# Kernel tuning notes

Measured on AMD Instinct MI355X. Metric: run time of the kernel, lower is better.

The kernel has to match this reference:

```python
import jax, jax.numpy as jnp
import numpy as np

B, T, C = 4, 2048, 1024
H, D = 16, 64
SCALE = D ** -0.5


def setup_inputs() -> dict:
    key = jax.random.key(0)
    ks = jax.random.split(key, 5)
    s = 0.02
    return {
        "hidden_states": jax.random.normal(ks[0], (B, T, C), dtype=jnp.float32),
        "attention_mask": jnp.ones((B, T), dtype=jnp.int32),
        "Wq": jax.random.normal(ks[1], (C, H * D), dtype=jnp.float32) * s,
        "Wk": jax.random.normal(ks[2], (C, H * D), dtype=jnp.float32) * s,
        "Wv": jax.random.normal(ks[3], (C, H * D), dtype=jnp.float32) * s,
        "Wo": jax.random.normal(ks[4], (H * D, C), dtype=jnp.float32) * s,
        "bo": jnp.zeros((C,), dtype=jnp.float32),
    }


def reference(hidden_states, attention_mask, Wq, Wk, Wv, Wo, bo):
    b, t, _ = hidden_states.shape
    # projections -> (B, H, T, D)
    q = (hidden_states @ Wq).reshape(b, t, H, D).transpose(0, 2, 1, 3)
    k = (hidden_states @ Wk).reshape(b, t, H, D).transpose(0, 2, 1, 3)
    v = (hidden_states @ Wv).reshape(b, t, H, D).transpose(0, 2, 1, 3)
    # scores (B, H, Tq, Tk)
    scores = jnp.einsum("bhqd,bhkd->bhqk", q, k) * SCALE
    mask = attention_mask[:, None, None, :]  # (B,1,1,T), dim==2 branch
    scores = jnp.where(mask == 0, -jnp.inf, scores)
    probs = jax.nn.softmax(scores, axis=-1)
    out = jnp.einsum("bhqk,bhkd->bhqd", probs, v)
    out = out.transpose(0, 2, 1, 3).reshape(b, t, H * D)
    return out @ Wo + bo
```

## Files before the change

kernel.cpp:

```cpp
#include <hip/hip_runtime.h>
#include <hip/hip_bf16.h>

#define B_ 4
#define T_ 2048
#define C_ 1024
#define H_ 16
#define D_ 64
#define SCALE_ 0.125f
#define L2E 1.4426950408889634f
#define SE (SCALE_ * L2E)

typedef __attribute__((ext_vector_type(8))) short bf16x8;
typedef __attribute__((ext_vector_type(4))) float f32x4;

__device__ __forceinline__ unsigned short f2bf(float f) {
    union { float f; unsigned u; } v; v.f = f;
    unsigned r = v.u + 0x7fff + ((v.u >> 16) & 1);
    return (unsigned short)(r >> 16);
}

__device__ __forceinline__ unsigned pk2bf(float a, float b) {
    __hip_bfloat162 t = __float22bfloat162_rn(make_float2(a, b));
    union { __hip_bfloat162 h; unsigned u; } c; c.h = t;
    return c.u;
}

__device__ __forceinline__ void gl_lds16(const unsigned short* g, unsigned short* l) {
    __builtin_amdgcn_global_load_lds(
        (const __attribute__((address_space(1))) void*)g,
        (__attribute__((address_space(3))) void*)l,
        16, 0, 0);
}

__global__ void cvt_hs_kernel(const float4* __restrict__ in, ushort4* __restrict__ out) {
    int i = blockIdx.x * 256 + threadIdx.x;
    float4 v = in[i];
    ushort4 o;
    o.x = f2bf(v.x); o.y = f2bf(v.y); o.z = f2bf(v.z); o.w = f2bf(v.w);
    out[i] = o;
}

__global__ void wtrans_kernel(const float* __restrict__ Wq, const float* __restrict__ Wk,
                              const float* __restrict__ Wv, const float* __restrict__ Wo,
                              unsigned short* __restrict__ Wqkv_t, unsigned short* __restrict__ Wo_t) {
    __shared__ float tile[64][65];
    int mtx = blockIdx.y;
    const float* W = (mtx == 0) ? Wq : (mtx == 1) ? Wk : (mtx == 2) ? Wv : Wo;
    unsigned short* Out = (mtx < 3) ? (Wqkv_t + (size_t)mtx * 1024 * 1024) : Wo_t;
    int tl = blockIdx.x;
    int tx = tl & 15, ty = tl >> 4;
    int t = threadIdx.x;
    int col = t & 63, rb = t >> 6;
#pragma unroll
    for (int rr = 0; rr < 16; ++rr) {
        int r = rb * 16 + rr;
        tile[r][col] = W[(size_t)(ty * 64 + r) * 1024 + tx * 64 + col];
    }
    __syncthreads();
#pragma unroll
    for (int rr = 0; rr < 16; ++rr) {
        int r = rb * 16 + rr;
        Out[(size_t)(tx * 64 + r) * 1024 + ty * 64 + col] = f2bf(tile[col][r]);
    }
}

__global__ __launch_bounds__(256) void gemm_qkv_kernel(
    const unsigned short* __restrict__ A, const unsigned short* __restrict__ Bt,
    unsigned short* __restrict__ Qg, unsigned short* __restrict__ Kf, unsigned short* __restrict__ Vf) {
    __shared__ __align__(16) unsigned short As[128 * 32];
    __shared__ __align__(16) unsigned short Bs[128 * 32];
    const int tid = threadIdx.x;
    const int w = tid >> 6, lane = tid & 63;
    const int quad = lane >> 4, l16 = lane & 15;
    const int m0 = blockIdx.y * 128, n0 = blockIdx.x * 128;
    const int mw = (w >> 1) * 64, nw = (w & 1) * 64;
    const int K = 1024;
    const int srow = lane >> 2;
    const int scol = (lane & 3) * 8;

    const f32x4 fzero = {0.f, 0.f, 0.f, 0.f};
    f32x4 acc[4][4];
#pragma unroll
    for (int i = 0; i < 4; ++i)
#pragma unroll
        for (int j = 0; j < 4; ++j) acc[i][j] = fzero;

    for (int k0 = 0; k0 < K; k0 += 32) {
        gl_lds16(A + (size_t)(m0 + w * 32 + srow) * K + k0 + scol,       As + (w * 32) * 32);
        gl_lds16(A + (size_t)(m0 + w * 32 + 16 + srow) * K + k0 + scol,  As + (w * 32 + 16) * 32);
        gl_lds16(Bt + (size_t)(n0 + w * 32 + srow) * K + k0 + scol,      Bs + (w * 32) * 32);
        gl_lds16(Bt + (size_t)(n0 + w * 32 + 16 + srow) * K + k0 + scol, Bs + (w * 32 + 16) * 32);
        __syncthreads();
        bf16x8 a[4], b[4];
#pragma unroll
        for (int i = 0; i < 4; ++i)
            a[i] = *(const bf16x8*)(As + (mw + i * 16 + l16) * 32 + quad * 8);
#pragma unroll
        for (int j = 0; j < 4; ++j)
            b[j] = *(const bf16x8*)(Bs + (nw + j * 16 + l16) * 32 + quad * 8);
#pragma unroll
        for (int i = 0; i < 4; ++i)
#pragma unroll
            for (int j = 0; j < 4; ++j)
                acc[i][j] = __builtin_amdgcn_mfma_f32_16x16x32_bf16(a[i], b[j], acc[i][j], 0, 0, 0);
        __syncthreads();
    }

#pragma unroll
    for (int j = 0; j < 4; ++j) {
        int gn = n0 + nw + j * 16 + l16;
        int tensor = gn >> 10;
        int nl = gn & 1023;
        int hh = nl >> 6, dd = nl & 63;
#pragma unroll
        for (int i = 0; i < 4; ++i) {
            int gmb = m0 + mw + i * 16 + quad * 4;
            int bb = gmb >> 11;
            size_t bhh = (size_t)(bb * 16 + hh);
            if (tensor == 0) {
#pragma unroll
                for (int r = 0; r < 4; ++r) {
                    int tt = (gmb + r) & 2047;
                    Qg[(bhh * 2048 + tt) * 64 + dd] = f2bf(acc[i][j][r] * SE);
                }
            } else if (tensor == 1) {
#pragma unroll
                for (int r = 0; r < 4; ++r) {
                    int tt = (gmb + r) & 2047;
                    Kf[bhh * 131072 + (size_t)(tt >> 4) * 1024 + (dd >> 5) * 512 +
                       (((dd >> 3) & 3) * 16 + (tt & 15)) * 8 + (dd & 7)] = f2bf(acc[i][j][r]);
                }
            } else {
                int tt = gmb & 2047;
                ushort4 v4;
                v4.x = f2bf(acc[i][j][0]); v4.y = f2bf(acc[i][j][1]);
                v4.z = f2bf(acc[i][j][2]); v4.w = f2bf(acc[i][j][3]);
                *(ushort4*)(Vf + bhh * 131072 + (size_t)(tt >> 5) * 2048 + (dd >> 4) * 512 +
                            (((tt >> 3) & 3) * 16 + (dd & 15)) * 8 + (tt & 7)) = v4;
            }
        }
    }
}

__global__ __launch_bounds__(256) void attn_kernel(
    const unsigned short* __restrict__ Qg, const unsigned short* __restrict__ Kf,
    const unsigned short* __restrict__ Vf, const int* __restrict__ mask,
    unsigned short* __restrict__ AO) {
    __shared__ __align__(16) unsigned short Pbuf[4][2048];

    const int tid = threadIdx.x;
    const int w = tid >> 6, lane = tid & 63;
    const int quad = lane >> 4, l16 = lane & 15;
    const int bid = blockIdx.x;
    const int bh = (bid & 7) * 8 + ((bid >> 7) & 7);
    const int qt = (bid >> 3) & 15;
    const int b = bh >> 4, h = bh & 15;
    const size_t bh_td = (size_t)bh * (2048 * 64);
    const int q0w = qt * 128 + w * 32;

    bf16x8 aq[2][2];
#pragma unroll
    for (int qi = 0; qi < 2; ++qi)
#pragma unroll
        for (int hh = 0; hh < 2; ++hh)
            aq[qi][hh] = *(const bf16x8*)(Qg + bh_td + (size_t)(q0w + qi * 16 + l16) * 64 + hh * 32 + quad * 8);

    const unsigned short* Kp = Kf + bh_td + lane * 8;
    const unsigned short* Vp = Vf + bh_td + lane * 8;
    const int* mrow = mask + b * 2048;

    bf16x8 vones;
#pragma unroll
    for (int i = 0; i < 8; ++i) vones[i] = (short)0x3F80;

    const f32x4 fzero = {0.f, 0.f, 0.f, 0.f};
    f32x4 po[2][4];
    f32x4 pl[2];
#pragma unroll
    for (int qi = 0; qi < 2; ++qi) {
        pl[qi] = fzero;
#pragma unroll
        for (int nd = 0; nd < 4; ++nd) po[qi][nd] = fzero;
    }

    for (int k0 = 0; k0 < 2048; k0 += 64) {
        const int tb = (k0 >> 4) * 1024;
        bf16x8 ka0[4], ka1[4];
#pragma unroll
        for (int kt = 0; kt < 4; ++kt) {
            ka0[kt] = *(const bf16x8*)(Kp + tb + kt * 1024);
            ka1[kt] = *(const bf16x8*)(Kp + tb + kt * 1024 + 512);
        }

        int mk = mrow[k0 + lane];
        bool allok = (__ballot(mk != 0) == 0xFFFFFFFFFFFFFFFFull);

        if (allok) {
#pragma unroll
            for (int kt = 0; kt < 4; ++kt) {
                int pidx = ((((kt & 1) << 1) | (quad >> 1)) * 16 + l16) * 8 + (quad & 1) * 4;
#pragma unroll
                for (int qi = 0; qi < 2; ++qi) {
                    f32x4 st = __builtin_amdgcn_mfma_f32_16x16x32_bf16(ka0[kt], aq[qi][0], fzero, 0, 0, 0);
                    st = __builtin_amdgcn_mfma_f32_16x16x32_bf16(ka1[kt], aq[qi][1], st, 0, 0, 0);
                    float p0 = __builtin_amdgcn_exp2f(st[0]);
                    float p1 = __builtin_amdgcn_exp2f(st[1]);
                    float p2 = __builtin_amdgcn_exp2f(st[2]);
                    float p3 = __builtin_amdgcn_exp2f(st[3]);
                    uint2 pk; pk.x = pk2bf(p0, p1); pk.y = pk2bf(p2, p3);
                    *(uint2*)(Pbuf[w] + (qi * 2 + (kt >> 1)) * 512 + pidx) = pk;
                }
            }
        } else {
#pragma unroll
            for (int kt = 0; kt < 4; ++kt) {
                int4 mv = *(const int4*)(mrow + k0 + kt * 16 + quad * 4);
                float mb0 = mv.x ? 0.f : -1e30f;
                float mb1 = mv.y ? 0.f : -1e30f;
                float mb2 = mv.z ? 0.f : -1e30f;
                float mb3 = mv.w ? 0.f : -1e30f;
                int pidx = ((((kt & 1) << 1) | (quad >> 1)) * 16 + l16) * 8 + (quad & 1) * 4;
#pragma unroll
                for (int qi = 0; qi < 2; ++qi) {
                    f32x4 st = __builtin_amdgcn_mfma_f32_16x16x32_bf16(ka0[kt], aq[qi][0], fzero, 0, 0, 0);
                    st = __builtin_amdgcn_mfma_f32_16x16x32_bf16(ka1[kt], aq[qi][1], st, 0, 0, 0);
                    float p0 = __builtin_amdgcn_exp2f(st[0] + mb0);
                    float p1 = __builtin_amdgcn_exp2f(st[1] + mb1);
                    float p2 = __builtin_amdgcn_exp2f(st[2] + mb2);
                    float p3 = __builtin_amdgcn_exp2f(st[3] + mb3);
                    uint2 pk; pk.x = pk2bf(p0, p1); pk.y = pk2bf(p2, p3);
                    *(uint2*)(Pbuf[w] + (qi * 2 + (kt >> 1)) * 512 + pidx) = pk;
                }
            }
        }

        bf16x8 bv[2][4];
#pragma unroll
        for (int c = 0; c < 2; ++c)
#pragma unroll
            for (int nd = 0; nd < 4; ++nd)
                bv[c][nd] = *(const bf16x8*)(Vp + ((k0 >> 5) + c) * 2048 + nd * 512);

        asm volatile("s_waitcnt lgkmcnt(0)" ::: "memory");

#pragma unroll
        for (int c = 0; c < 2; ++c)
#pragma unroll
            for (int qi = 0; qi < 2; ++qi) {
                bf16x8 ap = *(const bf16x8*)(Pbuf[w] + (qi * 2 + c) * 512 + lane * 8);
#pragma unroll
                for (int nd = 0; nd < 4; ++nd)
                    po[qi][nd] = __builtin_amdgcn_mfma_f32_16x16x32_bf16(ap, bv[c][nd], po[qi][nd], 0, 0, 0);
                pl[qi] = __builtin_amdgcn_mfma_f32_16x16x32_bf16(ap, vones, pl[qi], 0, 0, 0);
            }
    }

#pragma unroll
    for (int qi = 0; qi < 2; ++qi)
#pragma unroll
        for (int r = 0; r < 4; ++r) {
            float linv = __builtin_amdgcn_rcpf(pl[qi][r]);
            int q = q0w + qi * 16 + quad * 4 + r;
            size_t ob = (size_t)(b * 2048 + q) * 1024 + h * 64;
#pragma unroll
            for (int nd = 0; nd < 4; ++nd)
                AO[ob + nd * 16 + l16] = f2bf(po[qi][nd][r] * linv);
        }
}

__global__ __launch_bounds__(256) void gemm_out_kernel(
    const unsigned short* __restrict__ A, const unsigned short* __restrict__ Bt,
    const float* __restrict__ bo, float* __restrict__ out) {
    __shared__ __align__(16) unsigned short As[128 * 32];
    __shared__ __align__(16) unsigned short Bs[128 * 32];
    const int tid = threadIdx.x;
    const int w = tid >> 6, lane = tid & 63;
    const int quad = lane >> 4, l16 = lane & 15;
    const int m0 = blockIdx.y * 128, n0 = blockIdx.x * 128;
    const int mw = (w >> 1) * 64, nw = (w & 1) * 64;
    const int K = 1024;
    const int srow = lane >> 2;
    const int scol = (lane & 3) * 8;

    const f32x4 fzero = {0.f, 0.f, 0.f, 0.f};
    f32x4 acc[4][4];
#pragma unroll
    for (int i = 0; i < 4; ++i)
#pragma unroll
        for (int j = 0; j < 4; ++j) acc[i][j] = fzero;

    for (int k0 = 0; k0 < K; k0 += 32) {
        gl_lds16(A + (size_t)(m0 + w * 32 + srow) * K + k0 + scol,       As + (w * 32) * 32);
        gl_lds16(A + (size_t)(m0 + w * 32 + 16 + srow) * K + k0 + scol,  As + (w * 32 + 16) * 32);
        gl_lds16(Bt + (size_t)(n0 + w * 32 + srow) * K + k0 + scol,      Bs + (w * 32) * 32);
        gl_lds16(Bt + (size_t)(n0 + w * 32 + 16 + srow) * K + k0 + scol, Bs + (w * 32 + 16) * 32);
        __syncthreads();
        bf16x8 a[4], b[4];
#pragma unroll
        for (int i = 0; i < 4; ++i)
            a[i] = *(const bf16x8*)(As + (mw + i * 16 + l16) * 32 + quad * 8);
#pragma unroll
        for (int j = 0; j < 4; ++j)
            b[j] = *(const bf16x8*)(Bs + (nw + j * 16 + l16) * 32 + quad * 8);
#pragma unroll
        for (int i = 0; i < 4; ++i)
#pragma unroll
            for (int j = 0; j < 4; ++j)
                acc[i][j] = __builtin_amdgcn_mfma_f32_16x16x32_bf16(a[i], b[j], acc[i][j], 0, 0, 0);
        __syncthreads();
    }

#pragma unroll
    for (int j = 0; j < 4; ++j) {
        int gn = n0 + nw + j * 16 + l16;
        float bias = bo[gn];
#pragma unroll
        for (int i = 0; i < 4; ++i) {
            int gmb = m0 + mw + i * 16 + quad * 4;
#pragma unroll
            for (int r = 0; r < 4; ++r)
                out[(size_t)(gmb + r) * 1024 + gn] = acc[i][j][r] + bias;
        }
    }
}

extern "C" void kernel_launch(void* const* d_in, const int* in_sizes, int n_in,
                              void* d_out, int out_size, void* d_ws, size_t ws_size,
                              hipStream_t stream) {
    const float* hs  = (const float*)d_in[0];
    const int* mask  = (const int*)d_in[1];
    const float* Wq  = (const float*)d_in[2];
    const float* Wk  = (const float*)d_in[3];
    const float* Wv  = (const float*)d_in[4];
    const float* Wo  = (const float*)d_in[5];
    const float* bo  = (const float*)d_in[6];
    float* out = (float*)d_out;

    char* ws = (char*)d_ws;
    unsigned short* hs_bf = (unsigned short*)(ws);
    unsigned short* wqkv  = (unsigned short*)(ws + 16777216);
    unsigned short* wo_t  = (unsigned short*)(ws + 23068672);
    unsigned short* Qg    = (unsigned short*)(ws + 25165824);
    unsigned short* Kf    = (unsigned short*)(ws + 41943040);
    unsigned short* Vf    = (unsigned short*)(ws + 58720256);
    unsigned short* AO    = (unsigned short*)(ws + 75497472);

    cvt_hs_kernel<<<8192, 256, 0, stream>>>((const float4*)hs, (ushort4*)hs_bf);
    wtrans_kernel<<<dim3(256, 4), 256, 0, stream>>>(Wq, Wk, Wv, Wo, wqkv, wo_t);
    gemm_qkv_kernel<<<dim3(24, 64), 256, 0, stream>>>(hs_bf, wqkv, Qg, Kf, Vf);
    attn_kernel<<<1024, 256, 0, stream>>>(Qg, Kf, Vf, mask, AO);
    gemm_out_kernel<<<dim3(8, 64), 256, 0, stream>>>(AO, wo_t, bo, out);
}
```

Before: 294.5 us.

## Software-pipeline K loads with register double buffering and hoist mask check

Checks the whole attention mask row once up front. When no key is masked, the kernel runs a fast loop that prefetches the next K tile into a second register set while the current tile is computed, and issues the V loads before the QK MFMAs. It also raises wave priority around MFMA groups with s_setprio. This is meant to hide global load latency and drop the per-iteration ballot, at the cost of more registers and a duplicated code path. The final prefetch reads one tile past the end of K (k0+128 = 2048), which goes out of bounds for the last head.

```diff
diff --git a/kernel.cpp b/kernel.cpp
--- a/kernel.cpp
+++ b/kernel.cpp
@@ -142,6 +142,62 @@
     }
 }
 
+
+__device__ __forceinline__ void attn_step(
+    int k0, const unsigned short* __restrict__ Kp, const unsigned short* __restrict__ Vp,
+    unsigned short* Pw, const bf16x8 (&aq)[2][2],
+    const bf16x8 (&ka0)[4], const bf16x8 (&ka1)[4],
+    bf16x8 (&kn0)[4], bf16x8 (&kn1)[4], int next_tb,
+    const bf16x8& vones, f32x4 (&po)[2][4], f32x4 (&pl)[2],
+    int quad, int l16, int lane) {
+    bf16x8 bv[2][4];
+#pragma unroll
+    for (int c = 0; c < 2; ++c)
+#pragma unroll
+        for (int nd = 0; nd < 4; ++nd)
+            bv[c][nd] = *(const bf16x8*)(Vp + ((k0 >> 5) + c) * 2048 + nd * 512);
+#pragma unroll
+    for (int kt = 0; kt < 4; ++kt) {
+        kn0[kt] = *(const bf16x8*)(Kp + next_tb + kt * 1024);
+        kn1[kt] = *(const bf16x8*)(Kp + next_tb + kt * 1024 + 512);
+    }
+
+    const f32x4 fzero = {0.f, 0.f, 0.f, 0.f};
+    const int pbase = (quad >> 1) * 128 + l16 * 8 + (quad & 1) * 4;
+#pragma unroll
+    for (int kt = 0; kt < 4; ++kt) {
+        int pidx = pbase + (kt & 1) * 256;
+#pragma unroll
+        for (int qi = 0; qi < 2; ++qi) {
+            __builtin_amdgcn_s_setprio(1);
+            f32x4 st = __builtin_amdgcn_mfma_f32_16x16x32_bf16(ka0[kt], aq[qi][0], fzero, 0, 0, 0);
+            st = __builtin_amdgcn_mfma_f32_16x16x32_bf16(ka1[kt], aq[qi][1], st, 0, 0, 0);
+            __builtin_amdgcn_s_setprio(0);
+            float p0 = __builtin_amdgcn_exp2f(st[0]);
+            float p1 = __builtin_amdgcn_exp2f(st[1]);
+            float p2 = __builtin_amdgcn_exp2f(st[2]);
+            float p3 = __builtin_amdgcn_exp2f(st[3]);
+            uint2 pk; pk.x = pk2bf(p0, p1); pk.y = pk2bf(p2, p3);
+            *(uint2*)(Pw + (qi * 2 + (kt >> 1)) * 512 + pidx) = pk;
+        }
+    }
+
+    asm volatile("s_waitcnt lgkmcnt(0)" ::: "memory");
+
+#pragma unroll
+    for (int c = 0; c < 2; ++c)
+#pragma unroll
+        for (int qi = 0; qi < 2; ++qi) {
+            bf16x8 ap = *(const bf16x8*)(Pw + (qi * 2 + c) * 512 + lane * 8);
+            __builtin_amdgcn_s_setprio(1);
+#pragma unroll
+            for (int nd = 0; nd < 4; ++nd)
+                po[qi][nd] = __builtin_amdgcn_mfma_f32_16x16x32_bf16(ap, bv[c][nd], po[qi][nd], 0, 0, 0);
+            pl[qi] = __builtin_amdgcn_mfma_f32_16x16x32_bf16(ap, vones, pl[qi], 0, 0, 0);
+            __builtin_amdgcn_s_setprio(0);
+        }
+}
+
 __global__ __launch_bounds__(256) void attn_kernel(
     const unsigned short* __restrict__ Qg, const unsigned short* __restrict__ Kf,
     const unsigned short* __restrict__ Vf, const int* __restrict__ mask,
@@ -183,76 +239,100 @@
         for (int nd = 0; nd < 4; ++nd) po[qi][nd] = fzero;
     }
 
-    for (int k0 = 0; k0 < 2048; k0 += 64) {
-        const int tb = (k0 >> 4) * 1024;
-        bf16x8 ka0[4], ka1[4];
+    bool okl = true;
+#pragma unroll
+    for (int r = 0; r < 8; ++r) {
+        int4 m4 = *(const int4*)(mrow + r * 256 + lane * 4);
+        okl = okl && (m4.x != 0) && (m4.y != 0) && (m4.z != 0) && (m4.w != 0);
+    }
+    const bool all_ok = (__ballot(okl) == 0xFFFFFFFFFFFFFFFFull);
+
+    if (all_ok) {
+        bf16x8 kaA0[4], kaA1[4], kaB0[4], kaB1[4];
 #pragma unroll
         for (int kt = 0; kt < 4; ++kt) {
-            ka0[kt] = *(const bf16x8*)(Kp + tb + kt * 1024);
-            ka1[kt] = *(const bf16x8*)(Kp + tb + kt * 1024 + 512);
-        }
-
-        int mk = mrow[k0 + lane];
-        bool allok = (__ballot(mk != 0) == 0xFFFFFFFFFFFFFFFFull);
-
-        if (allok) {
+            kaA0[kt] = *(const bf16x8*)(Kp + kt * 1024);
+            kaA1[kt] = *(const bf16x8*)(Kp + kt * 1024 + 512);
+        }
+#pragma unroll 1
+        for (int k0 = 0; k0 < 2048; k0 += 128) {
+            attn_step(k0, Kp, Vp, Pbuf[w], aq, kaA0, kaA1, kaB0, kaB1,
+                      ((k0 + 64) >> 4) * 1024, vones, po, pl, quad, l16, lane);
+            attn_step(k0 + 64, Kp, Vp, Pbuf[w], aq, kaB0, kaB1, kaA0, kaA1,
+                      ((k0 + 128) >> 4) * 1024, vones, po, pl, quad, l16, lane);
+        }
+    } else {
+        for (int k0 = 0; k0 < 2048; k0 += 64) {
+            const int tb = (k0 >> 4) * 1024;
+            bf16x8 ka0[4], ka1[4];
 #pragma unroll
             for (int kt = 0; kt < 4; ++kt) {
-                int pidx = ((((kt & 1) << 1) | (quad >> 1)) * 16 + l16) * 8 + (quad & 1) * 4;
-#pragma unroll
-                for (int qi = 0; qi < 2; ++qi) {
-                    f32x4 st = __builtin_amdgcn_mfma_f32_16x16x32_bf16(ka0[kt], aq[qi][0], fzero, 0, 0, 0);
-                    st = __builtin_amdgcn_mfma_f32_16x16x32_bf16(ka1[kt], aq[qi][1], st, 0, 0, 0);
-                    float p0 = __builtin_amdgcn_exp2f(st[0]);
-                    float p1 = __builtin_amdgcn_exp2f(st[1]);
-                    float p2 = __builtin_amdgcn_exp2f(st[2]);
-                    float p3 = __builtin_amdgcn_exp2f(st[3]);
-                    uint2 pk; pk.x = pk2bf(p0, p1); pk.y = pk2bf(p2, p3);
-                    *(uint2*)(Pbuf[w] + (qi * 2 + (kt >> 1)) * 512 + pidx) = pk;
+                ka0[kt] = *(const bf16x8*)(Kp + tb + kt * 1024);
+                ka1[kt] = *(const bf16x8*)(Kp + tb + kt * 1024 + 512);
+            }
+
+            int mk = mrow[k0 + lane];
+            bool allok = (__ballot(mk != 0) == 0xFFFFFFFFFFFFFFFFull);
+
+            if (allok) {
+#pragma unroll
+                for (int kt = 0; kt < 4; ++kt) {
+                    int pidx = ((((kt & 1) << 1) | (quad >> 1)) * 16 + l16) * 8 + (quad & 1) * 4;
+#pragma unroll
+                    for (int qi = 0; qi < 2; ++qi) {
+                        f32x4 st = __builtin_amdgcn_mfma_f32_16x16x32_bf16(ka0[kt], aq[qi][0], fzero, 0, 0, 0);
+                        st = __builtin_amdgcn_mfma_f32_16x16x32_bf16(ka1[kt], aq[qi][1], st, 0, 0, 0);
+                        float p0 = __builtin_amdgcn_exp2f(st[0]);
+                        float p1 = __builtin_amdgcn_exp2f(st[1]);
+                        float p2 = __builtin_amdgcn_exp2f(st[2]);
+                        float p3 = __builtin_amdgcn_exp2f(st[3]);
+                        uint2 pk; pk.x = pk2bf(p0, p1); pk.y = pk2bf(p2, p3);
+                        *(uint2*)(Pbuf[w] + (qi * 2 + (kt >> 1)) * 512 + pidx) = pk;
+                    }
+                }
+            } else {
+#pragma unroll
+                for (int kt = 0; kt < 4; ++kt) {
+                    int4 mv = *(const int4*)(mrow + k0 + kt * 16 + quad * 4);
+                    float mb0 = mv.x ? 0.f : -1e30f;
+                    float mb1 = mv.y ? 0.f : -1e30f;
+                    float mb2 = mv.z ? 0.f : -1e30f;
+                    float mb3 = mv.w ? 0.f : -1e30f;
+                    int pidx = ((((kt & 1) << 1) | (quad >> 1)) * 16 + l16) * 8 + (quad & 1) * 4;
+#pragma unroll
+                    for (int qi = 0; qi < 2; ++qi) {
+                        f32x4 st = __builtin_amdgcn_mfma_f32_16x16x32_bf16(ka0[kt], aq[qi][0], fzero, 0, 0, 0);
+                        st = __builtin_amdgcn_mfma_f32_16x16x32_bf16(ka1[kt], aq[qi][1], st, 0, 0, 0);
+                        float p0 = __builtin_amdgcn_exp2f(st[0] + mb0);
+                        float p1 = __builtin_amdgcn_exp2f(st[1] + mb1);
+                        float p2 = __builtin_amdgcn_exp2f(st[2] + mb2);
+                        float p3 = __builtin_amdgcn_exp2f(st[3] + mb3);
+                        uint2 pk; pk.x = pk2bf(p0, p1); pk.y = pk2bf(p2, p3);
+                        *(uint2*)(Pbuf[w] + (qi * 2 + (kt >> 1)) * 512 + pidx) = pk;
+                    }
                 }
             }
-        } else {
-#pragma unroll
-            for (int kt = 0; kt < 4; ++kt) {
-                int4 mv = *(const int4*)(mrow + k0 + kt * 16 + quad * 4);
-                float mb0 = mv.x ? 0.f : -1e30f;
-                float mb1 = mv.y ? 0.f : -1e30f;
-                float mb2 = mv.z ? 0.f : -1e30f;
-                float mb3 = mv.w ? 0.f : -1e30f;
-                int pidx = ((((kt & 1) << 1) | (quad >> 1)) * 16 + l16) * 8 + (quad & 1) * 4;
+
+            bf16x8 bv[2][4];
+#pragma unroll
+            for (int c = 0; c < 2; ++c)
+#pragma unroll
+                for (int nd = 0; nd < 4; ++nd)
+                    bv[c][nd] = *(const bf16x8*)(Vp + ((k0 >> 5) + c) * 2048 + nd * 512);
+
+            asm volatile("s_waitcnt lgkmcnt(0)" ::: "memory");
+
+#pragma unroll
+            for (int c = 0; c < 2; ++c)
 #pragma unroll
                 for (int qi = 0; qi < 2; ++qi) {
-                    f32x4 st = __builtin_amdgcn_mfma_f32_16x16x32_bf16(ka0[kt], aq[qi][0], fzero, 0, 0, 0);
-                    st = __builtin_amdgcn_mfma_f32_16x16x32_bf16(ka1[kt], aq[qi][1], st, 0, 0, 0);
-                    float p0 = __builtin_amdgcn_exp2f(st[0] + mb0);
-                    float p1 = __builtin_amdgcn_exp2f(st[1] + mb1);
-                    float p2 = __builtin_amdgcn_exp2f(st[2] + mb2);
-                    float p3 = __builtin_amdgcn_exp2f(st[3] + mb3);
-                    uint2 pk; pk.x = pk2bf(p0, p1); pk.y = pk2bf(p2, p3);
-                    *(uint2*)(Pbuf[w] + (qi * 2 + (kt >> 1)) * 512 + pidx) = pk;
+                    bf16x8 ap = *(const bf16x8*)(Pbuf[w] + (qi * 2 + c) * 512 + lane * 8);
+#pragma unroll
+                    for (int nd = 0; nd < 4; ++nd)
+                        po[qi][nd] = __builtin_amdgcn_mfma_f32_16x16x32_bf16(ap, bv[c][nd], po[qi][nd], 0, 0, 0);
+                    pl[qi] = __builtin_amdgcn_mfma_f32_16x16x32_bf16(ap, vones, pl[qi], 0, 0, 0);
                 }
-            }
-        }
-
-        bf16x8 bv[2][4];
-#pragma unroll
-        for (int c = 0; c < 2; ++c)
-#pragma unroll
-            for (int nd = 0; nd < 4; ++nd)
-                bv[c][nd] = *(const bf16x8*)(Vp + ((k0 >> 5) + c) * 2048 + nd * 512);
-
-        asm volatile("s_waitcnt lgkmcnt(0)" ::: "memory");
-
-#pragma unroll
-        for (int c = 0; c < 2; ++c)
-#pragma unroll
-            for (int qi = 0; qi < 2; ++qi) {
-                bf16x8 ap = *(const bf16x8*)(Pbuf[w] + (qi * 2 + c) * 512 + lane * 8);
-#pragma unroll
-                for (int nd = 0; nd < 4; ++nd)
-                    po[qi][nd] = __builtin_amdgcn_mfma_f32_16x16x32_bf16(ap, bv[c][nd], po[qi][nd], 0, 0, 0);
-                pl[qi] = __builtin_amdgcn_mfma_f32_16x16x32_bf16(ap, vones, pl[qi], 0, 0, 0);
-            }
+        }
     }
 
 #pragma unroll
```

Result: slower. 304.5 us (+3.4%).

## Double-buffer K/V tiles in LDS and share them across 8 waves per block

Applied to the files above, without the earlier changes.

The attention kernel now uses 512-thread blocks covering 256 query rows, so eight waves share each K/V tile. Tiles are loaded into shared memory with direct global-to-LDS copies, and the next tile is prefetched into a second buffer while the current one is computed. Before, every wave read K and V straight from global memory. The aim is to cut redundant global/L2 traffic and hide load latency. In exchange it adds a block-wide barrier every 64 keys and more LDS per block, which may limit occupancy, and it halves the grid to 512 blocks.

```diff
diff --git a/kernel.cpp b/kernel.cpp
--- a/kernel.cpp
+++ b/kernel.cpp
@@ -142,21 +142,105 @@
     }
 }
 
-__global__ __launch_bounds__(256) void attn_kernel(
+__device__ __forceinline__ void attn_step_staged(
+    int k0, const unsigned short* Kc, const unsigned short* Vc,
+    unsigned short* Kn, unsigned short* Vn, int kn0,
+    const unsigned short* __restrict__ Kg, const unsigned short* __restrict__ Vg,
+    unsigned short* Pw, const bf16x8 (&aq)[2][2], const bf16x8& vones,
+    f32x4 (&po)[2][4], f32x4 (&pl)[2],
+    const int* __restrict__ mrow, int w, int lane, int quad, int l16) {
+
+    gl_lds16(Kg + (size_t)(kn0 >> 4) * 1024 + w * 512 + lane * 8, Kn + w * 512);
+    gl_lds16(Vg + (size_t)(kn0 >> 5) * 2048 + w * 512 + lane * 8, Vn + w * 512);
+
+    bf16x8 ka0[4], ka1[4];
+#pragma unroll
+    for (int kt = 0; kt < 4; ++kt) {
+        ka0[kt] = *(const bf16x8*)(Kc + kt * 1024 + lane * 8);
+        ka1[kt] = *(const bf16x8*)(Kc + kt * 1024 + 512 + lane * 8);
+    }
+
+    const f32x4 fzero = {0.f, 0.f, 0.f, 0.f};
+    int mk = mrow[k0 + lane];
+    bool allok = (__ballot(mk != 0) == 0xFFFFFFFFFFFFFFFFull);
+
+    if (allok) {
+#pragma unroll
+        for (int kt = 0; kt < 4; ++kt) {
+            int pidx = ((((kt & 1) << 1) | (quad >> 1)) * 16 + l16) * 8 + (quad & 1) * 4;
+#pragma unroll
+            for (int qi = 0; qi < 2; ++qi) {
+                f32x4 st = __builtin_amdgcn_mfma_f32_16x16x32_bf16(ka0[kt], aq[qi][0], fzero, 0, 0, 0);
+                st = __builtin_amdgcn_mfma_f32_16x16x32_bf16(ka1[kt], aq[qi][1], st, 0, 0, 0);
+                float p0 = __builtin_amdgcn_exp2f(st[0]);
+                float p1 = __builtin_amdgcn_exp2f(st[1]);
+                float p2 = __builtin_amdgcn_exp2f(st[2]);
+                float p3 = __builtin_amdgcn_exp2f(st[3]);
+                uint2 pk; pk.x = pk2bf(p0, p1); pk.y = pk2bf(p2, p3);
+                *(uint2*)(Pw + (qi * 2 + (kt >> 1)) * 512 + pidx) = pk;
+            }
+        }
+    } else {
+#pragma unroll
+        for (int kt = 0; kt < 4; ++kt) {
+            int4 mv = *(const int4*)(mrow + k0 + kt * 16 + quad * 4);
+            float mb0 = mv.x ? 0.f : -1e30f;
+            float mb1 = mv.y ? 0.f : -1e30f;
+            float mb2 = mv.z ? 0.f : -1e30f;
+            float mb3 = mv.w ? 0.f : -1e30f;
+            int pidx = ((((kt & 1) << 1) | (quad >> 1)) * 16 + l16) * 8 + (quad & 1) * 4;
+#pragma unroll
+            for (int qi = 0; qi < 2; ++qi) {
+                f32x4 st = __builtin_amdgcn_mfma_f32_16x16x32_bf16(ka0[kt], aq[qi][0], fzero, 0, 0, 0);
+                st = __builtin_amdgcn_mfma_f32_16x16x32_bf16(ka1[kt], aq[qi][1], st, 0, 0, 0);
+                float p0 = __builtin_amdgcn_exp2f(st[0] + mb0);
+                float p1 = __builtin_amdgcn_exp2f(st[1] + mb1);
+                float p2 = __builtin_amdgcn_exp2f(st[2] + mb2);
+                float p3 = __builtin_amdgcn_exp2f(st[3] + mb3);
+                uint2 pk; pk.x = pk2bf(p0, p1); pk.y = pk2bf(p2, p3);
+                *(uint2*)(Pw + (qi * 2 + (kt >> 1)) * 512 + pidx) = pk;
+            }
+        }
+    }
+
+    bf16x8 bv[2][4];
+#pragma unroll
+    for (int c = 0; c < 2; ++c)
+#pragma unroll
+        for (int nd = 0; nd < 4; ++nd)
+            bv[c][nd] = *(const bf16x8*)(Vc + c * 2048 + nd * 512 + lane * 8);
+
+    asm volatile("s_waitcnt lgkmcnt(0)" ::: "memory");
+
+#pragma unroll
+    for (int c = 0; c < 2; ++c)
+#pragma unroll
+        for (int qi = 0; qi < 2; ++qi) {
+            bf16x8 ap = *(const bf16x8*)(Pw + (qi * 2 + c) * 512 + lane * 8);
+#pragma unroll
+            for (int nd = 0; nd < 4; ++nd)
+                po[qi][nd] = __builtin_amdgcn_mfma_f32_16x16x32_bf16(ap, bv[c][nd], po[qi][nd], 0, 0, 0);
+            pl[qi] = __builtin_amdgcn_mfma_f32_16x16x32_bf16(ap, vones, pl[qi], 0, 0, 0);
+        }
+}
+
+__global__ __launch_bounds__(512, 4) void attn_kernel(
     const unsigned short* __restrict__ Qg, const unsigned short* __restrict__ Kf,
     const unsigned short* __restrict__ Vf, const int* __restrict__ mask,
     unsigned short* __restrict__ AO) {
-    __shared__ __align__(16) unsigned short Pbuf[4][2048];
+    __shared__ __align__(16) unsigned short KsA[4096], KsB[4096];
+    __shared__ __align__(16) unsigned short VsA[4096], VsB[4096];
+    __shared__ __align__(16) unsigned short Pbuf[8][2048];
 
     const int tid = threadIdx.x;
     const int w = tid >> 6, lane = tid & 63;
     const int quad = lane >> 4, l16 = lane & 15;
     const int bid = blockIdx.x;
-    const int bh = (bid & 7) * 8 + ((bid >> 7) & 7);
-    const int qt = (bid >> 3) & 15;
+    const int bh = (bid & 7) * 8 + ((bid >> 6) & 7);
+    const int qt = (bid >> 3) & 7;
     const int b = bh >> 4, h = bh & 15;
     const size_t bh_td = (size_t)bh * (2048 * 64);
-    const int q0w = qt * 128 + w * 32;
+    const int q0w = qt * 256 + w * 32;
 
     bf16x8 aq[2][2];
 #pragma unroll
@@ -165,8 +249,8 @@
         for (int hh = 0; hh < 2; ++hh)
             aq[qi][hh] = *(const bf16x8*)(Qg + bh_td + (size_t)(q0w + qi * 16 + l16) * 64 + hh * 32 + quad * 8);
 
-    const unsigned short* Kp = Kf + bh_td + lane * 8;
-    const unsigned short* Vp = Vf + bh_td + lane * 8;
+    const unsigned short* Kg = Kf + bh_td;
+    const unsigned short* Vg = Vf + bh_td;
     const int* mrow = mask + b * 2048;
 
     bf16x8 vones;
@@ -183,76 +267,21 @@
         for (int nd = 0; nd < 4; ++nd) po[qi][nd] = fzero;
     }
 
-    for (int k0 = 0; k0 < 2048; k0 += 64) {
-        const int tb = (k0 >> 4) * 1024;
-        bf16x8 ka0[4], ka1[4];
-#pragma unroll
-        for (int kt = 0; kt < 4; ++kt) {
-            ka0[kt] = *(const bf16x8*)(Kp + tb + kt * 1024);
-            ka1[kt] = *(const bf16x8*)(Kp + tb + kt * 1024 + 512);
-        }
-
-        int mk = mrow[k0 + lane];
-        bool allok = (__ballot(mk != 0) == 0xFFFFFFFFFFFFFFFFull);
-
-        if (allok) {
-#pragma unroll
-            for (int kt = 0; kt < 4; ++kt) {
-                int pidx = ((((kt & 1) << 1) | (quad >> 1)) * 16 + l16) * 8 + (quad & 1) * 4;
-#pragma unroll
-                for (int qi = 0; qi < 2; ++qi) {
-                    f32x4 st = __builtin_amdgcn_mfma_f32_16x16x32_bf16(ka0[kt], aq[qi][0], fzero, 0, 0, 0);
-                    st = __builtin_amdgcn_mfma_f32_16x16x32_bf16(ka1[kt], aq[qi][1], st, 0, 0, 0);
-                    float p0 = __builtin_amdgcn_exp2f(st[0]);
-                    float p1 = __builtin_amdgcn_exp2f(st[1]);
-                    float p2 = __builtin_amdgcn_exp2f(st[2]);
-                    float p3 = __builtin_amdgcn_exp2f(st[3]);
-                    uint2 pk; pk.x = pk2bf(p0, p1); pk.y = pk2bf(p2, p3);
-                    *(uint2*)(Pbuf[w] + (qi * 2 + (kt >> 1)) * 512 + pidx) = pk;
-                }
-            }
-        } else {
-#pragma unroll
-            for (int kt = 0; kt < 4; ++kt) {
-                int4 mv = *(const int4*)(mrow + k0 + kt * 16 + quad * 4);
-                float mb0 = mv.x ? 0.f : -1e30f;
-                float mb1 = mv.y ? 0.f : -1e30f;
-                float mb2 = mv.z ? 0.f : -1e30f;
-                float mb3 = mv.w ? 0.f : -1e30f;
-                int pidx = ((((kt & 1) << 1) | (quad >> 1)) * 16 + l16) * 8 + (quad & 1) * 4;
-#pragma unroll
-                for (int qi = 0; qi < 2; ++qi) {
-                    f32x4 st = __builtin_amdgcn_mfma_f32_16x16x32_bf16(ka0[kt], aq[qi][0], fzero, 0, 0, 0);
-                    st = __builtin_amdgcn_mfma_f32_16x16x32_bf16(ka1[kt], aq[qi][1], st, 0, 0, 0);
-                    float p0 = __builtin_amdgcn_exp2f(st[0] + mb0);
-                    float p1 = __builtin_amdgcn_exp2f(st[1] + mb1);
-                    float p2 = __builtin_amdgcn_exp2f(st[2] + mb2);
-                    float p3 = __builtin_amdgcn_exp2f(st[3] + mb3);
-                    uint2 pk; pk.x = pk2bf(p0, p1); pk.y = pk2bf(p2, p3);
-                    *(uint2*)(Pbuf[w] + (qi * 2 + (kt >> 1)) * 512 + pidx) = pk;
-                }
-            }
-        }
-
-        bf16x8 bv[2][4];
-#pragma unroll
-        for (int c = 0; c < 2; ++c)
-#pragma unroll
-            for (int nd = 0; nd < 4; ++nd)
-                bv[c][nd] = *(const bf16x8*)(Vp + ((k0 >> 5) + c) * 2048 + nd * 512);
-
-        asm volatile("s_waitcnt lgkmcnt(0)" ::: "memory");
-
-#pragma unroll
-        for (int c = 0; c < 2; ++c)
-#pragma unroll
-            for (int qi = 0; qi < 2; ++qi) {
-                bf16x8 ap = *(const bf16x8*)(Pbuf[w] + (qi * 2 + c) * 512 + lane * 8);
-#pragma unroll
-                for (int nd = 0; nd < 4; ++nd)
-                    po[qi][nd] = __builtin_amdgcn_mfma_f32_16x16x32_bf16(ap, bv[c][nd], po[qi][nd], 0, 0, 0);
-                pl[qi] = __builtin_amdgcn_mfma_f32_16x16x32_bf16(ap, vones, pl[qi], 0, 0, 0);
-            }
+    gl_lds16(Kg + w * 512 + lane * 8, KsA + w * 512);
+    gl_lds16(Vg + w * 512 + lane * 8, VsA + w * 512);
+    asm volatile("s_waitcnt vmcnt(0)" ::: "memory");
+    __syncthreads();
+
+#pragma unroll 1
+    for (int k0 = 0; k0 < 2048; k0 += 128) {
+        attn_step_staged(k0, KsA, VsA, KsB, VsB, k0 + 64,
+                         Kg, Vg, Pbuf[w], aq, vones, po, pl, mrow, w, lane, quad, l16);
+        asm volatile("s_waitcnt vmcnt(0)" ::: "memory");
+        __syncthreads();
+        attn_step_staged(k0 + 64, KsB, VsB, KsA, VsA, (k0 + 128) & 2047,
+                         Kg, Vg, Pbuf[w], aq, vones, po, pl, mrow, w, lane, quad, l16);
+        asm volatile("s_waitcnt vmcnt(0)" ::: "memory");
+        __syncthreads();
     }
 
 #pragma unroll
@@ -297,7 +326,7 @@
         __syncthreads();
         bf16x8 a[4], b[4];
 #pragma unroll
-        for (int i = 0; i < 4; ++i)
+    for (int i = 0; i < 4; ++i)
             a[i] = *(const bf16x8*)(As + (mw + i * 16 + l16) * 32 + quad * 8);
 #pragma unroll
         for (int j = 0; j < 4; ++j)
@@ -348,6 +377,6 @@
     cvt_hs_kernel<<<8192, 256, 0, stream>>>((const float4*)hs, (ushort4*)hs_bf);
     wtrans_kernel<<<dim3(256, 4), 256, 0, stream>>>(Wq, Wk, Wv, Wo, wqkv, wo_t);
     gemm_qkv_kernel<<<dim3(24, 64), 256, 0, stream>>>(hs_bf, wqkv, Qg, Kf, Vf);
-    attn_kernel<<<1024, 256, 0, stream>>>(Qg, Kf, Vf, mask, AO);
+    attn_kernel<<<512, 512, 0, stream>>>(Qg, Kf, Vf, mask, AO);
     gemm_out_kernel<<<dim3(8, 64), 256, 0, stream>>>(AO, wo_t, bo, out);
 }
```

Result: faster. 279.5 us (-5.1%).
